# Kernel tuning notes

Measured on AMD Instinct MI355X. Metric: run time of the kernel, lower is better.

## Reference

```python
import jax, jax.numpy as jnp
import numpy as np


def setup_inputs() -> dict:
    key = jax.random.key(0)
    ks = jax.random.split(key, 5)
    d_out, d_in = 4096, 4096
    r = min(d_out, d_in)
    B, T = 4, 2048
    x = jax.random.normal(ks[0], (B, T, d_in), dtype=jnp.float32)
    U = jax.random.normal(ks[1], (d_out, r), dtype=jnp.float32)
    S = jax.random.uniform(ks[2], (r,), dtype=jnp.float32)
    Vt = jax.random.normal(ks[3], (r, d_in), dtype=jnp.float32)
    epsilon = jnp.zeros((r,), dtype=jnp.float32)
    bias = jax.random.normal(ks[4], (d_out,), dtype=jnp.float32)
    return {"x": x, "U": U, "S": S, "Vt": Vt, "epsilon": epsilon, "bias": bias}


def reference(x, U, S, Vt, epsilon, bias):
    # w = U @ diag(S + epsilon) @ Vt  (diag folded as column scale of U)
    w = (U * (S + epsilon)[None, :]) @ Vt  # [d_out, d_in]
    # F.linear: y = x @ w.T + bias
    return jnp.einsum('btk,ok->bto', x, w) + bias
```

## Files before the change

kernel.cpp:

```cpp
#include <hip/hip_runtime.h>
#include <hip/hip_bf16.h>
#include <stdint.h>

typedef __attribute__((ext_vector_type(4))) float f32x4;
typedef __attribute__((ext_vector_type(8))) short short8v;

typedef __attribute__((address_space(1))) void gvoid;
typedef __attribute__((address_space(3))) void lvoid;

#define GLD16(gp, lp) __builtin_amdgcn_global_load_lds((const gvoid*)(gp), (lvoid*)(lp), 16, 0, 0)

__device__ __forceinline__ unsigned short f2bf(float f) {
    union { float ff; unsigned uu; } a; a.ff = f;
    unsigned u = a.uu;
    u += 0x7FFFu + ((u >> 16) & 1u);
    return (unsigned short)(u >> 16);
}

__global__ __launch_bounds__(256) void prep_u_kernel(
    const float* __restrict__ U, const float* __restrict__ S,
    const float* __restrict__ eps, unsigned short* __restrict__ Ub) {
    long idx = ((long)blockIdx.x * 256 + threadIdx.x) * 8;
    int r = (int)(idx & 4095);
    f32x4 u0 = *(const f32x4*)(U + idx);
    f32x4 u1 = *(const f32x4*)(U + idx + 4);
    f32x4 s0 = *(const f32x4*)(S + r);
    f32x4 s1 = *(const f32x4*)(S + r + 4);
    f32x4 e0 = *(const f32x4*)(eps + r);
    f32x4 e1 = *(const f32x4*)(eps + r + 4);
    union { uint4 v; unsigned short s[8]; } o;
#pragma unroll
    for (int j = 0; j < 4; ++j) {
        o.s[j]     = f2bf(u0[j] * (s0[j] + e0[j]));
        o.s[j + 4] = f2bf(u1[j] * (s1[j] + e1[j]));
    }
    *(uint4*)(Ub + idx) = o.v;
}

__global__ __launch_bounds__(256) void cvt_bf16_kernel(
    const float* __restrict__ src, unsigned short* __restrict__ dst) {
    long idx = ((long)blockIdx.x * 256 + threadIdx.x) * 8;
    f32x4 v0 = *(const f32x4*)(src + idx);
    f32x4 v1 = *(const f32x4*)(src + idx + 4);
    union { uint4 v; unsigned short s[8]; } o;
#pragma unroll
    for (int j = 0; j < 4; ++j) {
        o.s[j]     = f2bf(v0[j]);
        o.s[j + 4] = f2bf(v1[j]);
    }
    *(uint4*)(dst + idx) = o.v;
}

__global__ __launch_bounds__(256) void transpose_cvt_kernel(
    const float* __restrict__ src, unsigned short* __restrict__ dst) {
    __shared__ float tile[64][65];
    int tx = threadIdx.x & 63;
    int tq = threadIdx.x >> 6;
    int r0 = blockIdx.y << 6;
    int k0 = blockIdx.x << 6;
#pragma unroll
    for (int i = 0; i < 16; ++i) {
        int row = (i << 2) + tq;
        tile[row][tx] = src[(long)(r0 + row) * 4096 + k0 + tx];
    }
    __syncthreads();
#pragma unroll
    for (int i = 0; i < 16; ++i) {
        int krow = (i << 2) + tq;
        dst[(long)(k0 + krow) * 4096 + r0 + tx] = f2bf(tile[tx][krow]);
    }
}

#define MM(a, b, c) __builtin_amdgcn_mfma_f32_16x16x32_bf16(a, b, c, 0, 0, 0)

#define ACH(bf, kh) (As + ((bf) * 2 + (kh)) * 8192)
#define BCH(bf, kh) (Bs + ((bf) * 2 + (kh)) * 8192)

#define STAGE_A(bf, kh, koff) do { \
    const unsigned short* _s = A + gAr + (koff); \
    unsigned short* _d = ACH(bf, kh) + wave * 512; \
    GLD16(_s, _d); GLD16(_s + (long)128 * K, _d + 4096); } while (0)

#define STAGE_B(bf, kh, koff) do { \
    const unsigned short* _s = B + gBr + (koff); \
    unsigned short* _d = BCH(bf, kh) + wave * 512; \
    GLD16(_s, _d); GLD16(_s + (long)128 * K, _d + 4096); } while (0)

#define LOAD_A(bf, ks, mh) do { \
    const unsigned short* _p = ACH(bf, ks) + aBase + (mh) * 2048; \
    _Pragma("unroll") \
    for (int _m = 0; _m < 4; ++_m) aR[_m] = *(const short8v*)(_p + _m * 512); } while (0)

#define READ_B(bf, ks) do { \
    const unsigned short* _p = BCH(bf, ks) + bBase; \
    _Pragma("unroll") \
    for (int _n = 0; _n < 4; ++_n) bR[_n] = *(const short8v*)(_p + _n * 512); } while (0)

#define PH_SYNC do { \
    __builtin_amdgcn_s_barrier(); \
    asm volatile("s_waitcnt lgkmcnt(0)" ::: "memory"); \
    __builtin_amdgcn_sched_barrier(0); } while (0)

#define MFMA16(mh) do { \
    __builtin_amdgcn_s_setprio(1); \
    _Pragma("unroll") \
    for (int _m = 0; _m < 4; ++_m) { \
        acc[(mh) * 4 + _m][0] = MM(aR[_m], bR[0], acc[(mh) * 4 + _m][0]); \
        acc[(mh) * 4 + _m][1] = MM(aR[_m], bR[1], acc[(mh) * 4 + _m][1]); \
        acc[(mh) * 4 + _m][2] = MM(aR[_m], bR[2], acc[(mh) * 4 + _m][2]); \
        acc[(mh) * 4 + _m][3] = MM(aR[_m], bR[3], acc[(mh) * 4 + _m][3]); \
    } \
    __builtin_amdgcn_s_setprio(0); } while (0)

#define VM4 asm volatile("s_waitcnt vmcnt(4)" ::: "memory")
#define PH_END __builtin_amdgcn_s_barrier()

template<int OUT_BF16, int BIAS>
__global__ __launch_bounds__(512, 2) void gemm256_kernel(
    const unsigned short* __restrict__ A,
    const unsigned short* __restrict__ B,
    void* __restrict__ Cv, const float* __restrict__ bias,
    int M, int N, int K) {
    __shared__ unsigned short As[4 * 8192];
    __shared__ unsigned short Bs[4 * 8192];

    const int tid  = threadIdx.x;
    const int wave = tid >> 6;
    const int lane = tid & 63;
    const int fr   = lane & 15;
    const int fq   = lane >> 4;

    const int nwg = gridDim.x;
    const int bid = blockIdx.x;
    const int cpx = nwg >> 3;
    const int wg  = (bid & 7) * cpx + (bid >> 3);
    const int ntn = N >> 8;
    const long m0 = (long)(wg / ntn) << 8;
    const long n0 = (long)(wg % ntn) << 8;

    const int wwr = wave >> 2;
    const int wwc = wave & 3;

    const int  rS  = tid >> 2;
    const int  sS  = (tid & 3) ^ ((rS >> 1) & 3);
    const long gAr = (m0 + rS) * K + sS * 8;
    const long gBr = (n0 + rS) * K + sS * 8;

    const int swz   = (fq ^ ((fr >> 1) & 3)) * 8;
    const int aBase = (wwr * 128 + fr) * 32 + swz;
    const int bBase = (wwc * 64 + fr) * 32 + swz;

    f32x4  acc[8][4] = {};
    short8v aR[4], bR[4];

    STAGE_A(0, 0, 0);  STAGE_B(0, 0, 0);
    STAGE_A(0, 1, 32); STAGE_B(0, 1, 32);
    STAGE_A(1, 0, 64); STAGE_B(1, 0, 64);
    VM4;
    __builtin_amdgcn_s_barrier();

    const int nIter = K >> 7;
    for (int i = 0; i < nIter; ++i) {
        const int kt1off = 128 * i + 96;
        int k3 = 128 * i + 128; if (k3 >= K) k3 -= K;
        int k5 = 128 * i + 160; if (k5 >= K) k5 -= K;
        int k7 = 128 * i + 192; if (k7 >= K) k7 -= K;

        LOAD_A(0, 0, 0); READ_B(0, 0); STAGE_A(1, 1, kt1off);
        PH_SYNC; MFMA16(0); PH_END;
        LOAD_A(0, 0, 1); STAGE_B(1, 1, kt1off);
        PH_SYNC; MFMA16(1); PH_END;
        LOAD_A(0, 1, 0); READ_B(0, 1); STAGE_A(0, 0, k3);
        PH_SYNC; MFMA16(0); PH_END;
        LOAD_A(0, 1, 1); STAGE_B(0, 0, k3);
        PH_SYNC; MFMA16(1); VM4; PH_END;
        LOAD_A(1, 0, 0); READ_B(1, 0); STAGE_A(0, 1, k5);
        PH_SYNC; MFMA16(0); PH_END;
        LOAD_A(1, 0, 1); STAGE_B(0, 1, k5);
        PH_SYNC; MFMA16(1); PH_END;
        LOAD_A(1, 1, 0); READ_B(1, 1); STAGE_A(1, 0, k7);
        PH_SYNC; MFMA16(0); PH_END;
        LOAD_A(1, 1, 1); STAGE_B(1, 0, k7);
        PH_SYNC; MFMA16(1); VM4; PH_END;
    }

#pragma unroll
    for (int nf = 0; nf < 4; ++nf) {
        const int col = (int)n0 + wwc * 64 + nf * 16 + fr;
        float bv = BIAS ? bias[col] : 0.0f;
#pragma unroll
        for (int mf = 0; mf < 8; ++mf) {
            f32x4 v = acc[mf][nf];
            long rowb = m0 + wwr * 128 + mf * 16 + fq * 4;
#pragma unroll
            for (int j = 0; j < 4; ++j) {
                float val = v[j] + bv;
                long off = (rowb + j) * N + col;
                if (OUT_BF16) ((unsigned short*)Cv)[off] = f2bf(val);
                else          ((float*)Cv)[off] = val;
            }
        }
    }
}

extern "C" void kernel_launch(void* const* d_in, const int* in_sizes, int n_in,
                              void* d_out, int out_size, void* d_ws, size_t ws_size,
                              hipStream_t stream) {
    const float* x    = (const float*)d_in[0];
    const float* U    = (const float*)d_in[1];
    const float* S    = (const float*)d_in[2];
    const float* Vt   = (const float*)d_in[3];
    const float* eps  = (const float*)d_in[4];
    const float* bias = (const float*)d_in[5];
    float* out = (float*)d_out;

    char* ws = (char*)d_ws;
    unsigned short* Ub  = (unsigned short*)(ws);
    unsigned short* VtT = (unsigned short*)(ws + (size_t)(32 << 20));
    unsigned short* Wb  = (unsigned short*)(ws + (size_t)(64 << 20));
    unsigned short* Xb  = (unsigned short*)(ws);

    prep_u_kernel<<<8192, 256, 0, stream>>>(U, S, eps, Ub);
    transpose_cvt_kernel<<<dim3(64, 64), 256, 0, stream>>>(Vt, VtT);
    gemm256_kernel<1, 0><<<256, 512, 0, stream>>>(Ub, VtT, (void*)Wb, nullptr,
                                                  4096, 4096, 4096);
    cvt_bf16_kernel<<<16384, 256, 0, stream>>>(x, Xb);
    gemm256_kernel<0, 1><<<512, 512, 0, stream>>>(Xb, Wb, (void*)out, bias,
                                                  8192, 4096, 4096);
}
```

Measured before the change: 460.1 us.

## Switch GEMM inner loop to 32x32x16 bf16 MFMA with merged phases

Replaces the 16x16x32 MFMA tiling with 32x32x16 MFMAs. Each wave now holds 4x2 accumulator tiles of 16 floats and reads swizzled LDS fragments for two k-halves per phase. The eight sync phases per iteration are collapsed into four, each staging both A and B, with the vmcnt wait raised to 8. The goal is fewer LDS reads per flop and fewer barriers, at the cost of a different fragment layout, a new epilogue mapping and deeper outstanding loads.

```diff
diff --git a/kernel.cpp b/kernel.cpp
--- a/kernel.cpp
+++ b/kernel.cpp
@@ -2,8 +2,9 @@
 #include <hip/hip_bf16.h>
 #include <stdint.h>
 
-typedef __attribute__((ext_vector_type(4))) float f32x4;
-typedef __attribute__((ext_vector_type(8))) short short8v;
+typedef __attribute__((ext_vector_type(4)))  float f32x4;
+typedef __attribute__((ext_vector_type(16))) float f32x16;
+typedef __attribute__((ext_vector_type(8)))  short short8v;
 
 typedef __attribute__((address_space(1))) void gvoid;
 typedef __attribute__((address_space(3))) void lvoid;
@@ -71,7 +72,7 @@
     }
 }
 
-#define MM(a, b, c) __builtin_amdgcn_mfma_f32_16x16x32_bf16(a, b, c, 0, 0, 0)
+#define MM32(a, b, c) __builtin_amdgcn_mfma_f32_32x32x16_bf16(a, b, c, 0, 0, 0)
 
 #define ACH(bf, kh) (As + ((bf) * 2 + (kh)) * 8192)
 #define BCH(bf, kh) (Bs + ((bf) * 2 + (kh)) * 8192)
@@ -86,33 +87,37 @@
     unsigned short* _d = BCH(bf, kh) + wave * 512; \
     GLD16(_s, _d); GLD16(_s + (long)128 * K, _d + 4096); } while (0)
 
-#define LOAD_A(bf, ks, mh) do { \
-    const unsigned short* _p = ACH(bf, ks) + aBase + (mh) * 2048; \
-    _Pragma("unroll") \
-    for (int _m = 0; _m < 4; ++_m) aR[_m] = *(const short8v*)(_p + _m * 512); } while (0)
-
-#define READ_B(bf, ks) do { \
-    const unsigned short* _p = BCH(bf, ks) + bBase; \
-    _Pragma("unroll") \
-    for (int _n = 0; _n < 4; ++_n) bR[_n] = *(const short8v*)(_p + _n * 512); } while (0)
+#define LDA32(bf, kh) do { \
+    const unsigned short* _p = ACH(bf, kh) + aRowB; \
+    _Pragma("unroll") \
+    for (int _m = 0; _m < 4; ++_m) { \
+        aR[0][_m] = *(const short8v*)(_p + _m * 1024 + sl0); \
+        aR[1][_m] = *(const short8v*)(_p + _m * 1024 + sl1); } } while (0)
+
+#define LDB32(bf, kh) do { \
+    const unsigned short* _p = BCH(bf, kh) + bRowB; \
+    _Pragma("unroll") \
+    for (int _n = 0; _n < 2; ++_n) { \
+        bR[0][_n] = *(const short8v*)(_p + _n * 1024 + sl0); \
+        bR[1][_n] = *(const short8v*)(_p + _n * 1024 + sl1); } } while (0)
 
 #define PH_SYNC do { \
     __builtin_amdgcn_s_barrier(); \
     asm volatile("s_waitcnt lgkmcnt(0)" ::: "memory"); \
     __builtin_amdgcn_sched_barrier(0); } while (0)
 
-#define MFMA16(mh) do { \
+#define MFMA32 do { \
     __builtin_amdgcn_s_setprio(1); \
     _Pragma("unroll") \
+    for (int _ks = 0; _ks < 2; ++_ks) \
+    _Pragma("unroll") \
     for (int _m = 0; _m < 4; ++_m) { \
-        acc[(mh) * 4 + _m][0] = MM(aR[_m], bR[0], acc[(mh) * 4 + _m][0]); \
-        acc[(mh) * 4 + _m][1] = MM(aR[_m], bR[1], acc[(mh) * 4 + _m][1]); \
-        acc[(mh) * 4 + _m][2] = MM(aR[_m], bR[2], acc[(mh) * 4 + _m][2]); \
-        acc[(mh) * 4 + _m][3] = MM(aR[_m], bR[3], acc[(mh) * 4 + _m][3]); \
+        acc[_m][0] = MM32(aR[_ks][_m], bR[_ks][0], acc[_m][0]); \
+        acc[_m][1] = MM32(aR[_ks][_m], bR[_ks][1], acc[_m][1]); \
     } \
     __builtin_amdgcn_s_setprio(0); } while (0)
 
-#define VM4 asm volatile("s_waitcnt vmcnt(4)" ::: "memory")
+#define VM8 asm volatile("s_waitcnt vmcnt(8)" ::: "memory")
 #define PH_END __builtin_amdgcn_s_barrier()
 
 template<int OUT_BF16, int BIAS>
@@ -127,8 +132,8 @@
     const int tid  = threadIdx.x;
     const int wave = tid >> 6;
     const int lane = tid & 63;
-    const int fr   = lane & 15;
-    const int fq   = lane >> 4;
+    const int l5   = lane & 31;
+    const int hi   = lane >> 5;
 
     const int nwg = gridDim.x;
     const int bid = blockIdx.x;
@@ -146,56 +151,51 @@
     const long gAr = (m0 + rS) * K + sS * 8;
     const long gBr = (n0 + rS) * K + sS * 8;
 
-    const int swz   = (fq ^ ((fr >> 1) & 3)) * 8;
-    const int aBase = (wwr * 128 + fr) * 32 + swz;
-    const int bBase = (wwc * 64 + fr) * 32 + swz;
-
-    f32x4  acc[8][4] = {};
-    short8v aR[4], bR[4];
+    const int swz5 = (l5 >> 1) & 3;
+    const int sl0  = ((0 + hi) ^ swz5) * 8;
+    const int sl1  = ((2 + hi) ^ swz5) * 8;
+    const int aRowB = (wwr * 128 + l5) * 32;
+    const int bRowB = (wwc * 64 + l5) * 32;
+
+    f32x16  acc[4][2] = {};
+    short8v aR[2][4], bR[2][2];
 
     STAGE_A(0, 0, 0);  STAGE_B(0, 0, 0);
     STAGE_A(0, 1, 32); STAGE_B(0, 1, 32);
     STAGE_A(1, 0, 64); STAGE_B(1, 0, 64);
-    VM4;
+    VM8;
     __builtin_amdgcn_s_barrier();
 
     const int nIter = K >> 7;
     for (int i = 0; i < nIter; ++i) {
-        const int kt1off = 128 * i + 96;
+        const int kA = 128 * i + 96;
         int k3 = 128 * i + 128; if (k3 >= K) k3 -= K;
         int k5 = 128 * i + 160; if (k5 >= K) k5 -= K;
         int k7 = 128 * i + 192; if (k7 >= K) k7 -= K;
 
-        LOAD_A(0, 0, 0); READ_B(0, 0); STAGE_A(1, 1, kt1off);
-        PH_SYNC; MFMA16(0); PH_END;
-        LOAD_A(0, 0, 1); STAGE_B(1, 1, kt1off);
-        PH_SYNC; MFMA16(1); PH_END;
-        LOAD_A(0, 1, 0); READ_B(0, 1); STAGE_A(0, 0, k3);
-        PH_SYNC; MFMA16(0); PH_END;
-        LOAD_A(0, 1, 1); STAGE_B(0, 0, k3);
-        PH_SYNC; MFMA16(1); VM4; PH_END;
-        LOAD_A(1, 0, 0); READ_B(1, 0); STAGE_A(0, 1, k5);
-        PH_SYNC; MFMA16(0); PH_END;
-        LOAD_A(1, 0, 1); STAGE_B(0, 1, k5);
-        PH_SYNC; MFMA16(1); PH_END;
-        LOAD_A(1, 1, 0); READ_B(1, 1); STAGE_A(1, 0, k7);
-        PH_SYNC; MFMA16(0); PH_END;
-        LOAD_A(1, 1, 1); STAGE_B(1, 0, k7);
-        PH_SYNC; MFMA16(1); VM4; PH_END;
-    }
-
-#pragma unroll
-    for (int nf = 0; nf < 4; ++nf) {
-        const int col = (int)n0 + wwc * 64 + nf * 16 + fr;
+        LDA32(0, 0); LDB32(0, 0); STAGE_A(1, 1, kA); STAGE_B(1, 1, kA);
+        PH_SYNC; MFMA32; VM8; PH_END;
+        LDA32(0, 1); LDB32(0, 1); STAGE_A(0, 0, k3); STAGE_B(0, 0, k3);
+        PH_SYNC; MFMA32; VM8; PH_END;
+        LDA32(1, 0); LDB32(1, 0); STAGE_A(0, 1, k5); STAGE_B(0, 1, k5);
+        PH_SYNC; MFMA32; VM8; PH_END;
+        LDA32(1, 1); LDB32(1, 1); STAGE_A(1, 0, k7); STAGE_B(1, 0, k7);
+        PH_SYNC; MFMA32; VM8; PH_END;
+    }
+
+#pragma unroll
+    for (int nf = 0; nf < 2; ++nf) {
+        const int col = (int)n0 + wwc * 64 + nf * 32 + l5;
         float bv = BIAS ? bias[col] : 0.0f;
 #pragma unroll
-        for (int mf = 0; mf < 8; ++mf) {
-            f32x4 v = acc[mf][nf];
-            long rowb = m0 + wwr * 128 + mf * 16 + fq * 4;
-#pragma unroll
-            for (int j = 0; j < 4; ++j) {
-                float val = v[j] + bv;
-                long off = (rowb + j) * N + col;
+        for (int mf = 0; mf < 4; ++mf) {
+            f32x16 v = acc[mf][nf];
+            const long rb = m0 + wwr * 128 + mf * 32 + hi * 4;
+#pragma unroll
+            for (int r = 0; r < 16; ++r) {
+                long row = rb + (r & 3) + 8 * (r >> 2);
+                float val = v[r] + bv;
+                long off = row * N + col;
                 if (OUT_BF16) ((unsigned short*)Cv)[off] = f2bf(val);
                 else          ((float*)Cv)[off] = val;
             }
```

Result: slower. 503.6 us (+9.5%).
